# Performance work log

Hardware: AMD Instinct MI355X
Metric: run time of the kernel (lower is better)

Reference implementation:

```python
import jax, jax.numpy as jnp
import numpy as np
import math

# ---- module config (mirrors init_kwargs) ----
FRAME_H, FRAME_W = 480, 640
HFOV = 79.0
CAM_H_CM = 88.0            # camera_height * 100
NUM_SEM = 16
RES = 5                    # map_resolution (cm/cell)
MAP_SIZE_CM = 4800
DSC = 4                    # global_downscaling
DU = 4                     # du_scale
VR = 100                   # vision_range (cells)
CAT_THR, EXP_THR, MAP_THR = 5.0, 1.0, 1.0
MIN_D_CM, MAX_D_CM = 50.0, 350.0
NC = 6                     # MC.NON_SEM_CHANNELS
ML = MAP_SIZE_CM // DSC // RES   # 240 local map cells
MG = MAP_SIZE_CM // RES          # 960 global map cells
ZMIN = int(-40 / RES)            # -8
ZB = int(360 / RES) - ZMIN       # 80 z bins
MIN_MAP_H = int(25 / RES - ZMIN)            # 13
MAX_MAP_H = int((CAM_H_CM + 1) / RES - ZMIN)  # 25
BC_R = 200 // RES                # been-close radius (cells)
CENTER_POSE = (ML * RES) / 200.0 # agent start at local map center (m)


def _affine_grid(theta, H, W):
    # theta: (B,2,3); align_corners=True convention
    ys = jnp.linspace(-1.0, 1.0, H)
    xs = jnp.linspace(-1.0, 1.0, W)
    xg, yg = jnp.meshgrid(xs, ys)
    base = jnp.stack([xg, yg, jnp.ones_like(xg)], -1)  # (H,W,3)
    return jnp.einsum('bij,hwj->bhwi', theta, base)    # (B,H,W,2)


def _grid_sample(img, grid):
    # bilinear, align_corners=True, zero padding (matches F.grid_sample)
    B, C, H, W = img.shape
    x = (grid[..., 0] + 1.0) * 0.5 * (W - 1)
    y = (grid[..., 1] + 1.0) * 0.5 * (H - 1)
    x0, y0 = jnp.floor(x), jnp.floor(y)
    flat = img.reshape(B, C, H * W)
    out = jnp.zeros_like(img)
    for dx in (0.0, 1.0):
        for dy in (0.0, 1.0):
            xi, yi = x0 + dx, y0 + dy
            w = (1.0 - jnp.abs(x - xi)) * (1.0 - jnp.abs(y - yi))
            ok = (xi >= 0) & (xi <= W - 1) & (yi >= 0) & (yi <= H - 1)
            idx = (jnp.clip(yi, 0, H - 1).astype(jnp.int32) * W
                   + jnp.clip(xi, 0, W - 1).astype(jnp.int32))
            g = jnp.take_along_axis(flat, jnp.broadcast_to(idx.reshape(B, 1, -1), (B, C, H * W)), axis=2)
            out = out + g.reshape(B, C, H, W) * (w * ok)[:, None]
    return out


def _splat(gx, gy, gz, feat, valid):
    # trilinear scatter-add of per-point features into (VR,VR,ZB) voxel grid
    # gx,gy,gz,valid: (B,P); feat: (B,P,F)
    B, P = gx.shape
    F = feat.shape[-1]
    ncell = VR * VR * ZB
    acc = jnp.zeros((B * ncell, F), feat.dtype)
    base = (jnp.arange(B) * ncell)[:, None]
    x0, y0, z0 = jnp.floor(gx), jnp.floor(gy), jnp.floor(gz)
    for dx in (0.0, 1.0):
        for dy in (0.0, 1.0):
            for dz in (0.0, 1.0):
                xi, yi, zi = x0 + dx, y0 + dy, z0 + dz
                w = (1.0 - jnp.abs(gx - xi)) * (1.0 - jnp.abs(gy - yi)) * (1.0 - jnp.abs(gz - zi))
                ok = valid & (xi >= 0) & (xi < VR) & (yi >= 0) & (yi < VR) & (zi >= 0) & (zi < ZB)
                cell = (yi.astype(jnp.int32) * VR + xi.astype(jnp.int32)) * ZB + zi.astype(jnp.int32)
                idx = jnp.clip(base + cell, 0, B * ncell - 1).reshape(-1)
                upd = (feat * (w * ok.astype(feat.dtype))[..., None]).reshape(B * P, F)
                acc = acc.at[idx].add(upd)
    return acc.reshape(B, VR, VR, ZB, F).transpose(0, 4, 1, 2, 3)  # (B,F,VR,VR,ZB)


def _forward(seq_obs, seq_pose_delta, seq_camera_poses, init_local_map,
             init_global_map, init_local_pose, init_global_pose,
             init_lmb, init_origins, seq_dones, seq_update_global):
    B, T = seq_obs.shape[:2]
    C = NUM_SEM
    f = FRAME_W / (2.0 * math.tan(math.radians(HFOV) / 2.0))
    cx, cy = FRAME_W / 2.0, FRAME_H / 2.0
    xs = ((jnp.arange(0, FRAME_W, DU) - cx) / f).astype(jnp.float32)   # (Ws,)
    zr = ((cy - jnp.arange(0, FRAME_H, DU)) / f).astype(jnp.float32)   # (Hs,)
    # camera tilt (elevation) from extrinsics (identity -> 0)
    elev = jnp.arctan2(seq_camera_poses[:, 2, 1], seq_camera_poses[:, 2, 2])
    ce, se = jnp.cos(elev)[:, None, None], jnp.sin(elev)[:, None, None]
    Hs, Ws = FRAME_H // DU, FRAME_W // DU
    P = Hs * Ws
    row = jnp.arange(ML, dtype=jnp.float32)

    def step(carry, inp):
        local_map, global_map, pose = carry
        obs, pd, done, upd = inp
        done = done.astype(bool)
        upd = upd.astype(bool)
        # episode reset
        local_map = jnp.where(done[:, None, None, None], 0.0, local_map)
        global_map = jnp.where(done[:, None, None, None], 0.0, global_map)
        pose = jnp.where(done[:, None], jnp.array([CENTER_POSE, CENTER_POSE, 0.0], jnp.float32), pose)
        # pose update (get_new_pose_batch, degrees)
        tr = jnp.radians(pose[:, 2])
        nx = pose[:, 0] + pd[:, 0] * jnp.cos(tr) - pd[:, 1] * jnp.sin(tr)
        ny = pose[:, 1] + pd[:, 0] * jnp.sin(tr) + pd[:, 1] * jnp.cos(tr)
        nt = jnp.mod(pose[:, 2] + jnp.degrees(pd[:, 2]) + 180.0, 360.0) - 180.0
        pose = jnp.stack([nx, ny, nt], -1)
        # ---- depth -> egocentric point cloud (cm) ----
        d = obs[:, 3, ::DU, ::DU]                           # (B,Hs,Ws)
        valid = (d >= MIN_D_CM) & (d <= MAX_D_CM)
        lat = d * xs[None, None, :]
        up = d * zr[None, :, None]
        fwd = d * ce + up * se
        hgt = -d * se + up * ce + CAM_H_CM
        gx = (lat / RES + VR / 2.0).reshape(B, P)
        gy = (fwd / RES).reshape(B, P)
        gz = (hgt / RES - ZMIN).reshape(B, P)
        # features: occupancy + avg-pooled semantics (du_scale pooling)
        sem = obs[:, 4:].reshape(B, C, Hs, DU, Ws, DU).mean((3, 5))
        feat = jnp.concatenate([jnp.ones((B, 1, Hs, Ws), obs.dtype), sem], 1)
        feat = feat.reshape(B, 1 + C, P).transpose(0, 2, 1)  # (B,P,F)
        vox = _splat(gx, gy, gz, feat, valid.reshape(B, P))  # (B,F,VR,VR,ZB)
        agent_hp = vox[..., MIN_MAP_H:MAX_MAP_H].sum(-1)
        all_hp = vox.sum(-1)
        fp_map = jnp.clip(agent_hp[:, 0:1] / MAP_THR, 0.0, 1.0)
        fp_exp = jnp.clip(all_hp[:, 0:1] / EXP_THR, 0.0, 1.0)
        sem_pred = jnp.clip(agent_hp[:, 1:] / CAT_THR, 0.0, 1.0)
        agent_view = jnp.zeros((B, NC + C, ML, ML), obs.dtype)
        y1, x1 = ML // 2, ML // 2 - VR // 2
        agent_view = agent_view.at[:, 0:1, y1:y1 + VR, x1:x1 + VR].set(fp_map)
        agent_view = agent_view.at[:, 1:2, y1:y1 + VR, x1:x1 + VR].set(fp_exp)
        agent_view = agent_view.at[:, NC:, y1:y1 + VR, x1:x1 + VR].set(sem_pred)
        # ---- pose transform: rotation then translation grid_sample ----
        th = jnp.radians(90.0 - pose[:, 2])
        stx = -(pose[:, 0] * 100.0 / RES - ML / 2.0) / (ML / 2.0)
        sty = -(pose[:, 1] * 100.0 / RES - ML / 2.0) / (ML / 2.0)
        c, s = jnp.cos(th), jnp.sin(th)
        z0 = jnp.zeros_like(th)
        o1 = jnp.ones_like(th)
        th_rot = jnp.stack([jnp.stack([c, -s, z0], -1), jnp.stack([s, c, z0], -1)], 1)
        th_tr = jnp.stack([jnp.stack([o1, z0, stx], -1), jnp.stack([z0, o1, sty], -1)], 1)
        warped = _grid_sample(_grid_sample(agent_view, _affine_grid(th_rot, ML, ML)),
                              _affine_grid(th_tr, ML, ML))
        # dilate obstacle channel (3x3 ones kernel, 1 iter)
        obst = jax.lax.reduce_window(warped[:, 0:1], -jnp.inf, jax.lax.max,
                                     (1, 1, 3, 3), (1, 1, 1, 1), 'SAME')
        warped = warped.at[:, 0:1].set(obst)
        local_map = jnp.maximum(local_map, warped)
        # current location / visited / been-close disks
        acx, acy = pose[:, 0] * 100.0 / RES, pose[:, 1] * 100.0 / RES
        d2 = ((row[None, None, :] - acx[:, None, None]) ** 2
              + (row[None, :, None] - acy[:, None, None]) ** 2)
        curr = (d2 <= 4.0).astype(local_map.dtype)
        local_map = local_map.at[:, 2].set(curr)
        local_map = local_map.at[:, 3].max(curr)
        local_map = local_map.at[:, 4].max((d2 <= float(BC_R ** 2)).astype(local_map.dtype))
        # global map update at local map boundaries
        gnew = jax.vmap(lambda g, l, lm: jax.lax.dynamic_update_slice(g, l, (0, lm[0], lm[2])))(
            global_map, local_map, init_lmb)
        global_map = jnp.where(upd[:, None, None, None], gnew, global_map)
        gpose = pose + init_origins
        # map features: local NC ch + maxpooled global NC ch + local sem ch
        gmax = global_map[:, :NC].reshape(B, NC, MG // DSC, DSC, MG // DSC, DSC).max((3, 5))
        mf = jnp.concatenate([local_map[:, :NC], gmax, local_map[:, NC:]], 1)
        return (local_map, global_map, pose), (mf, pose, gpose)

    xs_t = (jnp.swapaxes(seq_obs, 0, 1), jnp.swapaxes(seq_pose_delta, 0, 1),
            jnp.swapaxes(seq_dones, 0, 1), jnp.swapaxes(seq_update_global, 0, 1))
    (fl, fg, _), (mfs, lps, gps) = jax.lax.scan(
        step, (init_local_map, init_global_map, init_local_pose), xs_t)
    seq_mf = jnp.swapaxes(mfs, 0, 1)
    seq_lp = jnp.swapaxes(lps, 0, 1)
    seq_gp = jnp.swapaxes(gps, 0, 1)
    seq_lmb = jnp.broadcast_to(init_lmb[:, None], (B, T, 4))
    seq_org = jnp.broadcast_to(init_origins[:, None], (B, T, 3))
    return seq_mf, fl, fg, seq_lp, seq_gp, seq_lmb, seq_org


def setup_inputs():
    key = jax.random.key(0)
    k0, k1 = jax.random.split(key)
    B, T = 4, 4
    obs = jax.random.uniform(k0, (B, T, 4 + NUM_SEM, FRAME_H, FRAME_W), jnp.float32)
    obs = obs.at[:, :, 3].set(MIN_D_CM + obs[:, :, 3] * (MAX_D_CM - MIN_D_CM))  # depth in cm
    obs = obs.at[:, :, 4:].set((obs[:, :, 4:] > 0.9).astype(jnp.float32))       # binary seg masks
    pd = jax.random.normal(k1, (B, T, 3), jnp.float32) * jnp.array([0.25, 0.05, 0.1], jnp.float32)
    lo = (MG - ML) // 2
    lmb = jnp.tile(jnp.array([[lo, lo + ML, lo, lo + ML]], jnp.int32), (B, 1))
    origins = jnp.concatenate([jnp.full((B, 2), lo * RES / 100.0, jnp.float32),
                               jnp.zeros((B, 1), jnp.float32)], 1)
    lp = jnp.concatenate([jnp.full((B, 2), CENTER_POSE, jnp.float32),
                          jnp.zeros((B, 1), jnp.float32)], 1)
    return {
        "seq_obs": obs,
        "seq_pose_delta": pd,
        "seq_camera_poses": jnp.broadcast_to(jnp.eye(4, dtype=jnp.float32), (B, 4, 4)),
        "init_local_map": jnp.zeros((B, NC + NUM_SEM, ML, ML), jnp.float32),
        "init_global_map": jnp.zeros((B, NC + NUM_SEM, MG, MG), jnp.float32),
        "init_local_pose": lp,
        "init_global_pose": lp + origins,
        "init_origins": origins,
        "seq_dones": jnp.zeros((B, T), jnp.int32),
        "seq_update_global": jnp.ones((B, T), jnp.int32),
        "init_lmb": lmb,
    }


def reference(seq_obs, seq_pose_delta, seq_camera_poses, init_local_map, init_global_map,
              init_local_pose, init_global_pose, init_origins, seq_dones,
              seq_update_global, init_lmb):
    return _forward(seq_obs, seq_pose_delta, seq_camera_poses, init_local_map,
                    init_global_map, init_local_pose, init_global_pose,
                    init_lmb, init_origins, seq_dones, seq_update_global)
```

## Files before the change

kernel.cpp:

```cpp
#include <hip/hip_runtime.h>
#include <math.h>

#ifndef M_PI
#define M_PI 3.14159265358979323846
#endif

#define BB 4
#define TT 4
#define NSEM 16
#define CHL 22
#define CHMF 28
#define ML 240
#define MG 960
#define VR 100
#define HS 120
#define WSW 160
#define NPL 18
#define CPAD 24
#define MLSQ (ML*ML)
#define MGSQ (MG*MG)
#define VRSQ (VR*VR)
#define PPT (HS*WSW)
#define NPART 12
#define PR 9
#define NGRP 5
#define NSPLAT (BB*TT*NPART*NGRP)

#define SZ_MF (BB*TT*CHMF*MLSQ)
#define SZ_FL (BB*CHL*MLSQ)
#define SZ_FG (BB*CHL*MGSQ)
#define OFF_FL SZ_MF
#define OFF_FG (OFF_FL + SZ_FL)
#define OFF_LP (OFF_FG + SZ_FG)
#define OFF_GP (OFF_LP + BB*TT*3)
#define OFF_LMB (OFF_GP + BB*TT*3)
#define OFF_ORG (OFF_LMB + BB*TT*4)

#define WS_SCAL 0
#define WS_FLAGS (WS_SCAL + BB*TT*8)
#define WS_AABB (WS_FLAGS + 4*BB)
#define WS_CACHE (WS_AABB + 4*BB*TT)
#define WS_PLANES (WS_CACHE + BB*6*MLSQ)
#define WS_I2 (WS_PLANES + BB*TT*VRSQ*CPAD)
#define PTSN (BB*TT*PPT)
#define WS_GY (WS_I2 + BB*TT*NPL*MLSQ)
#define WS_GX (WS_GY + PTSN)
#define WS_WZA (WS_GX + PTSN)
#define WS_WZL (WS_WZA + PTSN)
#define WS_SEMDS (WS_WZL + PTSN)

__global__ __launch_bounds__(256) void k_stage1(const float* __restrict__ obs,
                                                const float* __restrict__ cam,
                                                const float* __restrict__ pd,
                                                const float* __restrict__ ilp,
                                                const float* __restrict__ org,
                                                const int* __restrict__ lmb,
                                                const int* __restrict__ dones,
                                                const int* __restrict__ updg,
                                                float* __restrict__ out,
                                                float* __restrict__ ws)
{
    if (blockIdx.x == 0) {
        int i = threadIdx.x;
        if (i < BB*TT) {
            int b = i / TT, t = i % TT;
            for (int k = 0; k < 4; k++) out[OFF_LMB + (b*TT+t)*4 + k] = (float)lmb[b*4+k];
            for (int k = 0; k < 3; k++) out[OFF_ORG + (b*TT+t)*3 + k] = org[b*3+k];
        }
        if (i >= BB) return;
        int b = i;
        float p0 = ilp[b*3+0], p1 = ilp[b*3+1], p2 = ilp[b*3+2];
        const float D2R = 0.017453292519943295f;
        int lastDone = -1, lastUpd = -1;
        for (int t = 0; t < TT; t++) {
            if (dones[b*TT+t]) { p0 = 6.0f; p1 = 6.0f; p2 = 0.0f; lastDone = t; }
            if (updg[b*TT+t]) lastUpd = t;
            float tr = p2 * D2R;
            float c0 = cosf(tr), s0 = sinf(tr);
            float q0 = pd[(b*TT+t)*3+0], q1 = pd[(b*TT+t)*3+1], q2 = pd[(b*TT+t)*3+2];
            float nx = p0 + q0*c0 - q1*s0;
            float ny = p1 + q0*s0 + q1*c0;
            float a  = p2 + q2*57.29577951308232f + 180.0f;
            float m  = fmodf(a, 360.0f); if (m < 0.0f) m += 360.0f;
            float nt = m - 180.0f;
            p0 = nx; p1 = ny; p2 = nt;
            out[OFF_LP + (b*TT+t)*3+0] = nx;
            out[OFF_LP + (b*TT+t)*3+1] = ny;
            out[OFF_LP + (b*TT+t)*3+2] = nt;
            out[OFF_GP + (b*TT+t)*3+0] = nx + org[b*3+0];
            out[OFF_GP + (b*TT+t)*3+1] = ny + org[b*3+1];
            out[OFF_GP + (b*TT+t)*3+2] = nt + org[b*3+2];
            float th = (90.0f - nt) * D2R;
            float ax = nx*100.0f/5.0f, ay = ny*100.0f/5.0f;
            float cth = cosf(th), sth = sinf(th);
            float stxv = -(ax - 120.0f)/120.0f;
            float styv = -(ay - 120.0f)/120.0f;
            float* sc = ws + WS_SCAL + (b*TT+t)*8;
            sc[0] = cth;
            sc[1] = sth;
            sc[2] = stxv;
            sc[3] = styv;
            sc[4] = ax;
            sc[5] = ay;
            float imin = 1e9f, imax = -1e9f, jmin = 1e9f, jmax = -1e9f;
            #pragma unroll
            for (int q = 0; q < 4; q++) {
                float cx = (q & 1) ? 170.0f : 69.0f;
                float cy = (q & 2) ? 220.0f : 119.0f;
                float dj =  cth*(cx - 119.5f) + sth*(cy - 119.5f);
                float di = -sth*(cx - 119.5f) + cth*(cy - 119.5f);
                float jv = 119.5f + dj - stxv*119.5f;
                float iv = 119.5f + di - styv*119.5f;
                imin = fminf(imin, iv); imax = fmaxf(imax, iv);
                jmin = fminf(jmin, jv); jmax = fmaxf(jmax, jv);
            }
            float* ab = ws + WS_AABB + (b*TT+t)*4;
            ab[0] = floorf(imin) - 3.0f;
            ab[1] = ceilf(imax) + 3.0f;
            ab[2] = floorf(jmin) - 3.0f;
            ab[3] = ceilf(jmax) + 3.0f;
        }
        ws[WS_FLAGS + b*4 + 0] = (lastDone >= 0) ? 1.0f : 0.0f;
        ws[WS_FLAGS + b*4 + 1] = (lastUpd < lastDone) ? 1.0f : 0.0f;
        ws[WS_FLAGS + b*4 + 2] = (float)lastUpd;
        return;
    }
    int bb = blockIdx.x - 1;
    int bt = bb / 75;
    int b = bt / TT;
    int p = (bb % 75)*256 + threadIdx.x;
    int h = p / WSW, w = p % WSW;
    size_t pi = (size_t)bt*PPT + p;
    const float* ob = obs + (size_t)bt * 20 * 480 * 640;
    float d = ob[(size_t)(3*480 + 4*h)*640 + 4*w];
    if (!(d >= 50.0f && d <= 350.0f)) { ws[WS_GY + pi] = -1000.0f; return; }

    double fd = 640.0 / (2.0 * tan((79.0 * M_PI / 180.0) * 0.5));
    float ff  = (float)fd;
    float xsv = (float)(4*w - 320) / ff;
    float zrv = (240.0f - (float)(4*h)) / ff;
    float elev = atan2f(cam[b*16+9], cam[b*16+10]);
    float ce = cosf(elev), se = sinf(elev);
    float up  = d * zrv;
    float fwd = d*ce + up*se;
    float hgt = -d*se + up*ce + 88.0f;
    float gx = (d*xsv)/5.0f + 50.0f;
    float gy = fwd/5.0f;
    float gz = hgt/5.0f + 8.0f;

    float z0 = floorf(gz);
    float wza = 0.0f, wzl = 0.0f;
    #pragma unroll
    for (int dz = 0; dz < 2; dz++) {
        float zi = z0 + dz;
        float wz = 1.0f - fabsf(gz - zi);
        if (zi >= 0.0f && zi < 80.0f) {
            wzl += wz;
            if (zi >= 13.0f && zi < 25.0f) wza += wz;
        }
    }
    if (wzl == 0.0f && wza == 0.0f) { ws[WS_GY + pi] = -1000.0f; return; }

    ws[WS_GY + pi]  = gy;
    ws[WS_GX + pi]  = gx;
    ws[WS_WZA + pi] = wza;
    ws[WS_WZL + pi] = wzl;

    if (wza > 0.0f) {
        const float* sb = ob + (size_t)4*480*640 + (size_t)(4*h)*640 + 4*w;
        float* so = ws + WS_SEMDS + (size_t)bt*NSEM*PPT + p;
        #pragma unroll
        for (int k = 0; k < NSEM; k++) {
            float s = 0.0f;
            #pragma unroll
            for (int r = 0; r < 4; r++) {
                const float4 v = *(const float4*)(sb + (size_t)k*480*640 + r*640);
                s += v.x + v.y + v.z + v.w;
            }
            so[(size_t)k*PPT] = s * 0.0625f;
        }
    }
}

__global__ __launch_bounds__(256) void k_stage2(const float* __restrict__ igm,
                                                const int* __restrict__ dones,
                                                const int* __restrict__ lmb,
                                                float* __restrict__ planes,
                                                float* __restrict__ fg,
                                                float* __restrict__ out,
                                                float* __restrict__ ws)
{
    __shared__ float acc[4*PR*VR];
    int bid = blockIdx.x;
    if (bid < NSPLAT) {
        int bt = bid & 15;
        int part = (bid >> 4) % NPART;
        int grp = bid / (16*NPART);
        int rlo = part * PR;
        int c0  = (grp == 0) ? 0 : (2 + 4*(grp-1));
        int nch = (grp == 0) ? 2 : 4;
        for (int e = threadIdx.x; e < nch*PR*VR; e += 256) acc[e] = 0.0f;
        __syncthreads();

        const float* gyA  = ws + WS_GY  + (size_t)bt*PPT;
        const float* gxA  = ws + WS_GX  + (size_t)bt*PPT;
        const float* wzaA = ws + WS_WZA + (size_t)bt*PPT;
        const float* wzlA = ws + WS_WZL + (size_t)bt*PPT;
        const float* semA = ws + WS_SEMDS + (size_t)bt*NSEM*PPT + (size_t)(c0-2)*PPT;

        for (int p = threadIdx.x; p < PPT; p += 256) {
            float gy = gyA[p];
            float y0 = floorf(gy);
            if (y0 > (float)(rlo + PR - 1) || y0 + 1.0f < (float)rlo) continue;
            float wza = wzaA[p];
            if (grp != 0 && wza <= 0.0f) continue;
            float gx  = gxA[p];
            float x0 = floorf(gx);
            float sem[4];
            if (grp != 0) {
                #pragma unroll
                for (int k = 0; k < 4; k++) sem[k] = semA[(size_t)k*PPT + p];
            }
            float wzl = (grp == 0) ? wzlA[p] : 0.0f;
            #pragma unroll
            for (int dy = 0; dy < 2; dy++) {
                float yi = y0 + dy;
                if (!(yi >= 0.0f && yi < 100.0f)) continue;
                int r = (int)yi - rlo;
                if (r < 0 || r >= PR) continue;
                float wy = 1.0f - fabsf(gy - yi);
                #pragma unroll
                for (int dx = 0; dx < 2; dx++) {
                    float xi = x0 + dx;
                    if (!(xi >= 0.0f && xi < 100.0f)) continue;
                    float wxy = (1.0f - fabsf(gx - xi)) * wy;
                    if (wxy <= 0.0f) continue;
                    int cell = r*VR + (int)xi;
                    if (grp == 0) {
                        if (wza > 0.0f) atomicAdd(&acc[cell], wza*wxy);
                        if (wzl > 0.0f) atomicAdd(&acc[PR*VR + cell], wzl*wxy);
                    } else {
                        #pragma unroll
                        for (int k = 0; k < 4; k++) {
                            float sv = sem[k];
                            if (sv != 0.0f) atomicAdd(&acc[k*PR*VR + cell], sv*wza*wxy);
                        }
                    }
                }
            }
        }
        __syncthreads();

        int nrows = 100 - rlo; if (nrows > PR) nrows = PR;
        if (nrows <= 0) return;
        float* pl = planes + (size_t)bt*VRSQ*CPAD;
        for (int e = threadIdx.x; e < nch*nrows*VR; e += 256) {
            int c = e / (nrows*VR);
            int rc = e % (nrows*VR);
            int r = rc / VR, x = rc % VR;
            pl[(size_t)((rlo + r)*VR + x)*CPAD + (c0 + c)] = acc[c*PR*VR + r*VR + x];
        }
        return;
    }
    int fb = bid - NSPLAT;
    int blk = fb % 225;
    int c = (fb / 225) % CHL;
    int b = fb / (225*CHL);
    int idx = blk*256 + threadIdx.x;
    int i = idx / ML, j = idx % ML;
    bool anyDone = ws[WS_FLAGS + b*4 + 0] > 0.5f;
    bool zeroWin = ws[WS_FLAGS + b*4 + 1] > 0.5f;
    int lastUpd  = (int)ws[WS_FLAGS + b*4 + 2];
    int y0 = lmb[b*4+0], x0 = lmb[b*4+2];
    int iy0 = y0 >> 2, ix0 = x0 >> 2;
    bool inWin = (i >= iy0) && (i < iy0 + ML/4) && (j >= ix0) && (j < ix0 + ML/4);

    size_t base = ((size_t)b*CHL + c)*MGSQ + (size_t)(4*i)*MG + 4*j;
    const float* g = igm + base;
    float* go = fg + base;

    int act;
    if (inWin) act = zeroWin ? 1 : ((lastUpd >= 0) ? 2 : (anyDone ? 1 : 0));
    else       act = anyDone ? 1 : 0;

    if (c < 6) {
        float m = -3.0e38f;
        #pragma unroll
        for (int r = 0; r < 4; r++) {
            float4 q = *(const float4*)(g + (size_t)r*MG);
            if (act == 0) *(float4*)(go + (size_t)r*MG) = q;
            else if (act == 1) *(float4*)(go + (size_t)r*MG) = make_float4(0,0,0,0);
            m = fmaxf(m, fmaxf(fmaxf(q.x, q.y), fmaxf(q.z, q.w)));
        }
        ws[WS_CACHE + ((size_t)b*6 + c)*MLSQ + idx] = m;
        if (!inWin) {
            float v = m;
            for (int t = 0; t < TT; t++) {
                if (dones[b*TT+t]) v = 0.0f;
                out[(size_t)(b*TT+t)*CHMF*MLSQ + (6+c)*MLSQ + idx] = v;
            }
        }
    } else {
        if (act == 2) return;
        if (act == 1) {
            float4 z = make_float4(0,0,0,0);
            #pragma unroll
            for (int r = 0; r < 4; r++) *(float4*)(go + (size_t)r*MG) = z;
        } else {
            #pragma unroll
            for (int r = 0; r < 4; r++)
                *(float4*)(go + (size_t)r*MG) = *(const float4*)(g + (size_t)r*MG);
        }
    }
}

__global__ __launch_bounds__(256) void k_gs(const float* __restrict__ planes,
                                            const float* __restrict__ ws,
                                            float* __restrict__ I2)
{
    int bt = blockIdx.z;
    const float* ab = ws + WS_AABB + bt*4;
    int ilo = (int)ab[0], ihi = (int)ab[1], jlo = (int)ab[2], jhi = (int)ab[3];
    int r0 = blockIdx.y*16, q0 = blockIdx.x*16;
    if (r0+15 < ilo-2 || r0 > ihi+2 || q0+15 < jlo-2 || q0 > jhi+2) return;

    int i = r0 + (threadIdx.x >> 4);
    int j = q0 + (threadIdx.x & 15);
    int idx = i*ML + j;
    const float* sc = ws + WS_SCAL + bt*8;
    float c = sc[0], s = sc[1], stx = sc[2], sty = sc[3];
    float* o = I2 + (size_t)bt*NPL*MLSQ + idx;
    const float* pl = planes + (size_t)bt*VRSQ*CPAD;

    int   soff[16];
    float sw[16];
    float wsum = 0.0f;
    {
        float xg = (float)j * (float)(2.0/239.0) - 1.0f + stx;
        float yg = (float)i * (float)(2.0/239.0) - 1.0f + sty;
        float x = (xg + 1.0f)*0.5f*239.0f;
        float y = (yg + 1.0f)*0.5f*239.0f;
        float x0 = floorf(x), y0 = floorf(y);
        #pragma unroll
        for (int dy = 0; dy < 2; dy++) {
            float yi = y0 + dy;
            bool vy = (yi >= 0.0f && yi <= 239.0f);
            float wy = 1.0f - fabsf(y - yi);
            #pragma unroll
            for (int dx = 0; dx < 2; dx++) {
                float xi = x0 + dx;
                bool vx = (xi >= 0.0f && xi <= 239.0f);
                float w2v = (vy && vx) ? (1.0f - fabsf(x - xi)) * wy : 0.0f;
                int ci = (dy*2 + dx)*4;
                float xg1 = (float)(int)xi * (float)(2.0/239.0) - 1.0f;
                float yg1 = (float)(int)yi * (float)(2.0/239.0) - 1.0f;
                float gxr = c*xg1 - s*yg1;
                float gyr = s*xg1 + c*yg1;
                float xx = (gxr + 1.0f)*0.5f*239.0f;
                float yy = (gyr + 1.0f)*0.5f*239.0f;
                float xx0 = floorf(xx), yy0 = floorf(yy);
                #pragma unroll
                for (int dy1 = 0; dy1 < 2; dy1++) {
                    float syi = yy0 + dy1;
                    bool v1y = (syi >= 120.0f && syi < 220.0f);
                    float wy1 = 1.0f - fabsf(yy - syi);
                    #pragma unroll
                    for (int dx1 = 0; dx1 < 2; dx1++) {
                        float sxi = xx0 + dx1;
                        bool v1 = v1y && (sxi >= 70.0f && sxi < 170.0f);
                        float w1v = v1 ? (1.0f - fabsf(xx - sxi)) * wy1 : 0.0f;
                        float wt = w2v * w1v;
                        soff[ci + dy1*2 + dx1] = v1 ? ((int)syi - 120)*VR + ((int)sxi - 70) : 0;
                        sw[ci + dy1*2 + dx1] = wt;
                        wsum += wt;
                    }
                }
            }
        }
    }

    if (wsum <= 0.0f) {
        #pragma unroll
        for (int cc = 0; cc < NPL; cc++) o[(size_t)cc*MLSQ] = 0.0f;
        return;
    }
    float acc[NPL];
    #pragma unroll
    for (int cc = 0; cc < NPL; cc++) acc[cc] = 0.0f;
    #pragma unroll
    for (int k = 0; k < 16; k++) {
        float w = sw[k];
        if (w == 0.0f) continue;
        const float* pb = pl + (size_t)soff[k]*CPAD;
        float4 a0 = *(const float4*)(pb + 0);
        float4 a1 = *(const float4*)(pb + 4);
        float4 a2 = *(const float4*)(pb + 8);
        float4 a3 = *(const float4*)(pb + 12);
        float2 a4 = *(const float2*)(pb + 16);
        acc[0]  += fminf(a0.x, 1.0f) * w;
        acc[1]  += fminf(a0.y, 1.0f) * w;
        acc[2]  += fminf(a0.z / 5.0f, 1.0f) * w;
        acc[3]  += fminf(a0.w / 5.0f, 1.0f) * w;
        acc[4]  += fminf(a1.x / 5.0f, 1.0f) * w;
        acc[5]  += fminf(a1.y / 5.0f, 1.0f) * w;
        acc[6]  += fminf(a1.z / 5.0f, 1.0f) * w;
        acc[7]  += fminf(a1.w / 5.0f, 1.0f) * w;
        acc[8]  += fminf(a2.x / 5.0f, 1.0f) * w;
        acc[9]  += fminf(a2.y / 5.0f, 1.0f) * w;
        acc[10] += fminf(a2.z / 5.0f, 1.0f) * w;
        acc[11] += fminf(a2.w / 5.0f, 1.0f) * w;
        acc[12] += fminf(a3.x / 5.0f, 1.0f) * w;
        acc[13] += fminf(a3.y / 5.0f, 1.0f) * w;
        acc[14] += fminf(a3.z / 5.0f, 1.0f) * w;
        acc[15] += fminf(a3.w / 5.0f, 1.0f) * w;
        acc[16] += fminf(a4.x / 5.0f, 1.0f) * w;
        acc[17] += fminf(a4.y / 5.0f, 1.0f) * w;
    }
    #pragma unroll
    for (int cc = 0; cc < NPL; cc++) o[(size_t)cc*MLSQ] = acc[cc];
}

__global__ __launch_bounds__(256) void k_updl7(const float* __restrict__ I2,
                                               const float* __restrict__ ws,
                                               const float* __restrict__ ilm,
                                               const int* __restrict__ dones,
                                               const int* __restrict__ updg,
                                               const int* __restrict__ lmb,
                                               float* __restrict__ fl,
                                               float* __restrict__ fg,
                                               float* __restrict__ out)
{
    int bz = blockIdx.z;
    int b = bz / 7, g = bz % 7;
    int gi = blockIdx.y;
    int bx = blockIdx.x;
    int lane = threadIdx.x & 63, wv = threadIdx.x >> 6;
    int j0 = (bx < 3) ? bx*64 : 176;
    int j = j0 + lane;
    int i = gi*4 + wv;
    int idx = i*ML + j;

    int ncl, cl[4];
    switch (g) {
        case 0:  ncl = 1; cl[0] = 0; cl[1] = 0; cl[2] = 0; cl[3] = 0; break;
        case 1:  ncl = 3; cl[0] = 1; cl[1] = 2; cl[2] = 3; cl[3] = 0; break;
        case 2:  ncl = 2; cl[0] = 4; cl[1] = 5; cl[2] = 0; cl[3] = 0; break;
        default: ncl = 4; { int cc0 = 6 + (g-3)*4;
                 cl[0] = cc0; cl[1] = cc0+1; cl[2] = cc0+2; cl[3] = cc0+3; } break;
    }
    bool hasG = (g <= 2);

    __shared__ float red[4][3][16];

    const float* lmsrc = ilm + (size_t)b*CHL*MLSQ;
    float* lm = fl + (size_t)b*CHL*MLSQ;
    int y0 = lmb[b*4+0], x0 = lmb[b*4+2];
    bool zeroWin = ws[WS_FLAGS + b*4 + 1] > 0.5f;
    int lastUpd = (int)ws[WS_FLAGS + b*4 + 2];

    float S[4];
    #pragma unroll
    for (int q = 0; q < 4; q++) {
        int c = cl[q];
        S[q] = (q < ncl && c != 2) ? lmsrc[c*MLSQ + idx] : 0.0f;
    }

    bool writer = hasG && (wv == 0) && ((lane & 3) == 0);
    int cx = lane >> 2;
    int cellY = (y0 >> 2) + gi;
    int cellX = (x0 >> 2) + (j0 >> 2) + cx;
    float W[3];
    if (writer) {
        #pragma unroll
        for (int q = 0; q < 3; q++)
            if (q < ncl)
                W[q] = ws[WS_CACHE + ((size_t)b*6 + cl[q])*MLSQ + cellY*ML + cellX];
    }

    for (int t = 0; t < TT; t++) {
        int bt = b*TT + t;
        bool done = dones[bt] != 0;
        bool upd  = updg[bt] != 0;
        const float* src = I2 + (size_t)bt*NPL*MLSQ;
        float* mf = out + (size_t)bt*CHMF*MLSQ;
        const float* ab = ws + WS_AABB + bt*4;
        int ilo = (int)ab[0], ihi = (int)ab[1], jlo = (int)ab[2], jhi = (int)ab[3];
        bool inA = (i >= ilo) && (i <= ihi) && (j >= jlo) && (j <= jhi);

        float pooled = 0.0f;
        if (g == 0) {
            bool inP = (i >= ilo-1) && (i <= ihi+1) && (j >= jlo-1) && (j <= jhi+1);
            if (inP) {
                pooled = -3.0e38f;
                for (int di = -1; di <= 1; di++) {
                    int ii = i + di; if (ii < 0 || ii >= ML) continue;
                    for (int dj = -1; dj <= 1; dj++) {
                        int jj = j + dj; if (jj < 0 || jj >= ML) continue;
                        pooled = fmaxf(pooled, src[ii*ML + jj]);
                    }
                }
            }
        }
        const float* sc = ws + WS_SCAL + bt*8;
        float acx = sc[4], acy = sc[5];
        float ddx = (float)j - acx, ddy = (float)i - acy;
        float d2 = ddx*ddx + ddy*ddy;
        float curr = (d2 <= 4.0f) ? 1.0f : 0.0f;
        float bc   = (d2 <= 1600.0f) ? 1.0f : 0.0f;

        size_t goff = (size_t)(y0+i)*MG + (x0+j);
        bool wrG = (t == lastUpd) && !zeroWin;

        #pragma unroll
        for (int q = 0; q < 4; q++) {
            if (q >= ncl) continue;
            int c = cl[q];
            if (done) S[q] = 0.0f;
            float nv;
            if      (c == 0) nv = fmaxf(S[q], pooled);
            else if (c == 1) nv = fmaxf(S[q], inA ? src[MLSQ + idx] : 0.0f);
            else if (c == 2) nv = curr;
            else if (c == 3) nv = fmaxf(S[q], curr);
            else if (c == 4) nv = fmaxf(S[q], bc);
            else if (c == 5) nv = S[q];
            else             nv = fmaxf(S[q], inA ? src[(size_t)(c-4)*MLSQ + idx] : 0.0f);
            S[q] = nv;
            mf[(size_t)(c < 6 ? c : c + 6)*MLSQ + idx] = nv;
            if (wrG) fg[((size_t)b*CHL + c)*MGSQ + goff] = nv;
        }

        if (hasG) {
            #pragma unroll
            for (int q = 0; q < 3; q++) {
                if (q >= ncl) continue;
                float v = S[q];
                v = fmaxf(v, __shfl_xor(v, 1, 64));
                v = fmaxf(v, __shfl_xor(v, 2, 64));
                if ((lane & 3) == 0) red[wv][q][cx] = v;
            }
            __syncthreads();
            if (writer) {
                #pragma unroll
                for (int q = 0; q < 3; q++) {
                    if (q >= ncl) continue;
                    if (done) W[q] = 0.0f;
                    if (upd)  W[q] = fmaxf(fmaxf(red[0][q][cx], red[1][q][cx]),
                                           fmaxf(red[2][q][cx], red[3][q][cx]));
                    mf[(size_t)(6 + cl[q])*MLSQ + cellY*ML + cellX] = W[q];
                }
            }
            __syncthreads();
        }
    }
    #pragma unroll
    for (int q = 0; q < 4; q++)
        if (q < ncl) lm[(size_t)cl[q]*MLSQ + idx] = S[q];
}

extern "C" void kernel_launch(void* const* d_in, const int* in_sizes, int n_in,
                              void* d_out, int out_size, void* d_ws, size_t ws_size,
                              hipStream_t stream)
{
    const float* obs   = (const float*)d_in[0];
    const float* pd    = (const float*)d_in[1];
    const float* cam   = (const float*)d_in[2];
    const float* ilm   = (const float*)d_in[3];
    const float* igm   = (const float*)d_in[4];
    const float* ilp   = (const float*)d_in[5];
    const float* org   = (const float*)d_in[7];
    const int*   dones = (const int*)d_in[8];
    const int*   updg  = (const int*)d_in[9];
    const int*   lmb   = (const int*)d_in[10];
    float* out = (float*)d_out;
    float* ws  = (float*)d_ws;

    float* fl     = out + OFF_FL;
    float* fg     = out + OFF_FG;
    float* planes = ws + WS_PLANES;
    float* I2v    = ws + WS_I2;

    k_stage1<<<1 + 75*BB*TT, 256, 0, stream>>>(obs, cam, pd, ilp, org, lmb,
                                               dones, updg, out, ws);
    k_stage2<<<NSPLAT + 225*CHL*BB, 256, 0, stream>>>(igm, dones, lmb,
                                                      planes, fg, out, ws);
    k_gs<<<dim3(15, 15, BB*TT), 256, 0, stream>>>(planes, ws, I2v);
    k_updl7<<<dim3(4, 60, BB*7), 256, 0, stream>>>(I2v, ws, ilm, dones, updg, lmb,
                                                   fl, fg, out);
}
```

Before: 336.9 us.

## Remap wave tiles to 4x16 and reduce pooled cells via shuffles without LDS barriers

Each wave now covers a 4-row by 16-column tile instead of one 64-wide row, so the 4x4 max-pool for the downscaled map can be done entirely with cross-lane shuffles. This removes the shared-memory staging and both __syncthreads per timestep. All per-timestep source reads (pooling and inA loads) are also hoisted into a preloop, so loads for all timesteps can issue before the sequential update chain. In exchange, global accesses become 16-float segments per row instead of 64-wide coalesced rows, and register pressure rises.

```diff
diff --git a/kernel.cpp b/kernel.cpp
--- a/kernel.cpp
+++ b/kernel.cpp
@@ -434,10 +434,12 @@
     int b = bz / 7, g = bz % 7;
     int gi = blockIdx.y;
     int bx = blockIdx.x;
-    int lane = threadIdx.x & 63, wv = threadIdx.x >> 6;
-    int j0 = (bx < 3) ? bx*64 : 176;
-    int j = j0 + lane;
-    int i = gi*4 + wv;
+    int wv = threadIdx.x >> 6, lane = threadIdx.x & 63;
+    int jt = (bx < 3) ? bx*64 : 176;
+    int j0 = jt + wv*16;
+    int r  = lane >> 4, cc = lane & 15;
+    int i = gi*4 + r;
+    int j = j0 + cc;
     int idx = i*ML + j;
 
     int ncl, cl[4];
@@ -450,8 +452,6 @@
     }
     bool hasG = (g <= 2);
 
-    __shared__ float red[4][3][16];
-
     const float* lmsrc = ilm + (size_t)b*CHL*MLSQ;
     float* lm = fl + (size_t)b*CHL*MLSQ;
     int y0 = lmb[b*4+0], x0 = lmb[b*4+2];
@@ -465,10 +465,9 @@
         S[q] = (q < ncl && c != 2) ? lmsrc[c*MLSQ + idx] : 0.0f;
     }
 
-    bool writer = hasG && (wv == 0) && ((lane & 3) == 0);
-    int cx = lane >> 2;
+    bool writer = hasG && (r == 0) && ((cc & 3) == 0);
     int cellY = (y0 >> 2) + gi;
-    int cellX = (x0 >> 2) + (j0 >> 2) + cx;
+    int cellX = (x0 >> 2) + (j0 >> 2) + (cc >> 2);
     float W[3];
     if (writer) {
         #pragma unroll
@@ -477,30 +476,45 @@
                 W[q] = ws[WS_CACHE + ((size_t)b*6 + cl[q])*MLSQ + cellY*ML + cellX];
     }
 
+    float gv[TT][4];
+    #pragma unroll
+    for (int t = 0; t < TT; t++) {
+        int bt = b*TT + t;
+        const float* src = I2 + (size_t)bt*NPL*MLSQ;
+        const float* ab = ws + WS_AABB + bt*4;
+        int ilo = (int)ab[0], ihi = (int)ab[1], jlo = (int)ab[2], jhi = (int)ab[3];
+        bool inA = (i >= ilo) && (i <= ihi) && (j >= jlo) && (j <= jhi);
+        gv[t][0] = 0.0f; gv[t][1] = 0.0f; gv[t][2] = 0.0f; gv[t][3] = 0.0f;
+        if (g == 0) {
+            bool inP = (i >= ilo-1) && (i <= ihi+1) && (j >= jlo-1) && (j <= jhi+1);
+            if (inP) {
+                float m = -3.0e38f;
+                for (int di = -1; di <= 1; di++) {
+                    int ii = i + di; if (ii < 0 || ii >= ML) continue;
+                    for (int dj = -1; dj <= 1; dj++) {
+                        int jj = j + dj; if (jj < 0 || jj >= ML) continue;
+                        m = fmaxf(m, src[ii*ML + jj]);
+                    }
+                }
+                gv[t][0] = m;
+            }
+        } else if (g == 1) {
+            if (inA) gv[t][0] = src[MLSQ + idx];
+        } else if (g >= 3) {
+            if (inA) {
+                #pragma unroll
+                for (int q = 0; q < 4; q++)
+                    gv[t][q] = src[(size_t)(cl[q]-4)*MLSQ + idx];
+            }
+        }
+    }
+
+    #pragma unroll
     for (int t = 0; t < TT; t++) {
         int bt = b*TT + t;
         bool done = dones[bt] != 0;
         bool upd  = updg[bt] != 0;
-        const float* src = I2 + (size_t)bt*NPL*MLSQ;
         float* mf = out + (size_t)bt*CHMF*MLSQ;
-        const float* ab = ws + WS_AABB + bt*4;
-        int ilo = (int)ab[0], ihi = (int)ab[1], jlo = (int)ab[2], jhi = (int)ab[3];
-        bool inA = (i >= ilo) && (i <= ihi) && (j >= jlo) && (j <= jhi);
-
-        float pooled = 0.0f;
-        if (g == 0) {
-            bool inP = (i >= ilo-1) && (i <= ihi+1) && (j >= jlo-1) && (j <= jhi+1);
-            if (inP) {
-                pooled = -3.0e38f;
-                for (int di = -1; di <= 1; di++) {
-                    int ii = i + di; if (ii < 0 || ii >= ML) continue;
-                    for (int dj = -1; dj <= 1; dj++) {
-                        int jj = j + dj; if (jj < 0 || jj >= ML) continue;
-                        pooled = fmaxf(pooled, src[ii*ML + jj]);
-                    }
-                }
-            }
-        }
         const float* sc = ws + WS_SCAL + bt*8;
         float acx = sc[4], acy = sc[5];
         float ddx = (float)j - acx, ddy = (float)i - acy;
@@ -517,13 +531,13 @@
             int c = cl[q];
             if (done) S[q] = 0.0f;
             float nv;
-            if      (c == 0) nv = fmaxf(S[q], pooled);
-            else if (c == 1) nv = fmaxf(S[q], inA ? src[MLSQ + idx] : 0.0f);
+            if      (c == 0) nv = fmaxf(S[q], gv[t][0]);
+            else if (c == 1) nv = fmaxf(S[q], gv[t][0]);
             else if (c == 2) nv = curr;
             else if (c == 3) nv = fmaxf(S[q], curr);
             else if (c == 4) nv = fmaxf(S[q], bc);
             else if (c == 5) nv = S[q];
-            else             nv = fmaxf(S[q], inA ? src[(size_t)(c-4)*MLSQ + idx] : 0.0f);
+            else             nv = fmaxf(S[q], gv[t][q]);
             S[q] = nv;
             mf[(size_t)(c < 6 ? c : c + 6)*MLSQ + idx] = nv;
             if (wrG) fg[((size_t)b*CHL + c)*MGSQ + goff] = nv;
@@ -536,20 +550,14 @@
                 float v = S[q];
                 v = fmaxf(v, __shfl_xor(v, 1, 64));
                 v = fmaxf(v, __shfl_xor(v, 2, 64));
-                if ((lane & 3) == 0) red[wv][q][cx] = v;
-            }
-            __syncthreads();
-            if (writer) {
-                #pragma unroll
-                for (int q = 0; q < 3; q++) {
-                    if (q >= ncl) continue;
+                v = fmaxf(v, __shfl_xor(v, 16, 64));
+                v = fmaxf(v, __shfl_xor(v, 32, 64));
+                if (writer) {
                     if (done) W[q] = 0.0f;
-                    if (upd)  W[q] = fmaxf(fmaxf(red[0][q][cx], red[1][q][cx]),
-                                           fmaxf(red[2][q][cx], red[3][q][cx]));
+                    if (upd)  W[q] = v;
                     mf[(size_t)(6 + cl[q])*MLSQ + cellY*ML + cellX] = W[q];
                 }
             }
-            __syncthreads();
         }
     }
     #pragma unroll
```

New measurement: 327.1 us, median of 2. 1.03x faster.
